# Kernel optimization log

Hardware: AMD Instinct MI355X
Metric: run time of the kernel (lower is better)

Reference implementation:

```python
import jax, jax.numpy as jnp
import numpy as np

# Conv2d_mvm config (matches init_kwargs): the bit-sliced crossbar MVM is a
# fixed-point emulation of an exact stride-1 conv2d with padding=1, no bias.
C_IN, C_OUT, K, H, W, PAD = 16, 16, 3, 1024, 1024, 1


def setup_inputs() -> dict:
    key = jax.random.key(0)
    kx, kw = jax.random.split(key)
    x = jax.random.normal(kx, (1, C_IN, H, W), dtype=jnp.float32)
    # kaiming_uniform-style init for the conv weight
    fan_in = C_IN * K * K
    bound = 1.0 / np.sqrt(fan_in)
    weight = jax.random.uniform(kw, (C_OUT, C_IN, K, K), dtype=jnp.float32,
                                minval=-bound, maxval=bound)
    return {"x": x, "weight": weight}


def reference(x, weight):
    # Ideal math of the bit-sliced crossbar MVM: per output pixel, the
    # flattened (C_in*K*K) receptive field dotted with each flattened filter.
    out = jax.lax.conv_general_dilated(
        x, weight,
        window_strides=(1, 1),
        padding=((PAD, PAD), (PAD, PAD)),
        dimension_numbers=("NCHW", "OIHW", "NCHW"),
    )
    # Original forward returns (C_out, H_out, W_out) with batch=1 assumed.
    return out[0]
```

## Files before the change

kernel.cpp:

```cpp
#include <hip/hip_runtime.h>


#define H 1024
#define W 1024
#define HW (H * W)
#define TW 64
#define TH 8
#define NT 2
#define LROWS 10
#define LPITCH 2112
#define LDS_BYTES (LROWS * LPITCH)

typedef __bf16 bf16x8 __attribute__((ext_vector_type(8)));
typedef float f32x4 __attribute__((ext_vector_type(4)));
typedef unsigned short ushort8 __attribute__((ext_vector_type(8)));
typedef unsigned int uint4v __attribute__((ext_vector_type(4)));

__device__ __host__ inline unsigned short f2bf(float f) {
  unsigned u = __builtin_bit_cast(unsigned, f);
  return (unsigned short)((u + 0x7fffu + ((u >> 16) & 1u)) >> 16);
}

__global__ __launch_bounds__(256) void conv_prep(const float* __restrict__ w,
                                                 unsigned short* __restrict__ wA) {
  int i = blockIdx.x * 256 + threadIdx.x;
  if (i >= 5 * 64 * 8) return;
  int j = i & 7;
  int l = (i >> 3) & 63;
  int p = i >> 9;
  int k = (l >> 4) * 8 + j;
  int t = 2 * p + (k >> 4);
  int ci = k & 15;
  int co = l & 15;
  float v = (t <= 8) ? w[co * 144 + ci * 9 + t] : 0.f;
  wA[i] = f2bf(v);
}

__global__ __launch_bounds__(256, 4) void conv_mfma(
    const float* __restrict__ x, const unsigned short* __restrict__ wA,
    float* __restrict__ out) {
  __shared__ __align__(16) char lds[LDS_BYTES];

  const int tid  = threadIdx.x;
  const int lane = tid & 63;
  const int wave = tid >> 6;
  const int m = lane & 15;
  const int q = lane >> 4;
  const int colbase  = blockIdx.x * TW;
  const int rowbase0 = blockIdx.y * (TH * NT);

  const bool stager = tid < 180;
  int ly = 0;
  const float* xcol = x;
  float cmask[4];
  int lok[4], lb[4];
  if (stager) {
    ly = tid / 18;
    const int qx  = tid - ly * 18;
    const int gx0 = colbase - 4 + 4 * qx;
    const int gx0c = gx0 < 0 ? 0 : (gx0 > W - 4 ? W - 4 : gx0);
    xcol = x + gx0c;
#pragma unroll
    for (int i = 0; i < 4; ++i) {
      const int gx = gx0 + i;
      cmask[i] = ((unsigned)gx < (unsigned)W) ? 1.f : 0.f;
      const int lx = gx - (colbase - 1);
      lok[i] = (unsigned)lx < 66u;
      const int b = ly * LPITCH + lx * 32;
      lb[i] = b ^ (((lx >> 2) & 3) << 4);
    }
  }

  f32x4 L[16];
  float rowm;
  {
    const int gy = rowbase0 - 1 + ly;
    rowm = ((unsigned)gy < (unsigned)H) ? 1.f : 0.f;
    const int gyc = gy < 0 ? 0 : (gy > H - 1 ? H - 1 : gy);
    const float* xb = xcol + gyc * W;
    if (stager) {
#pragma unroll
      for (int c = 0; c < 16; ++c)
        L[c] = *(const f32x4*)(xb + c * HW);
    }
  }

  ushort8 wU[5];
#pragma unroll
  for (int p = 0; p < 5; ++p)
    wU[p] = *(const ushort8*)&wA[(p * 64 + lane) * 8];

  int baseaddr[5];
#pragma unroll
  for (int p = 0; p < 5; ++p) {
    int t = 2 * p + (q >> 1);
    int ky = 0, kx = 0;
    if (t <= 8) { ky = t / 3; kx = t - ky * 3; }
    int col = m + kx;
    int b = ky * LPITCH + col * 32 + (q & 1) * 16;
    b ^= ((col >> 2) & 3) << 4;
    baseaddr[p] = b + wave * 2 * LPITCH;
  }

#pragma unroll
  for (int t = 0; t < NT; ++t) {
    if (stager) {
#pragma unroll
      for (int h = 0; h < 2; ++h) {
#pragma unroll
        for (int i = 0; i < 4; ++i) {
          if (lok[i]) {
            const float fm = rowm * cmask[i];
            uint4v d;
#pragma unroll
            for (int p = 0; p < 4; ++p) {
              const unsigned lo = f2bf(L[h * 8 + 2 * p][i] * fm);
              const unsigned hi = f2bf(L[h * 8 + 2 * p + 1][i] * fm);
              d[p] = lo | (hi << 16);
            }
            *(uint4v*)(lds + (lb[i] ^ (h << 4)));
            *(uint4v*)(lds + (lb[i] ^ (h << 4))) = d;
          }
        }
      }
    }

    if (t + 1 < NT) {
      const int gy = rowbase0 + (t + 1) * TH - 1 + ly;
      const float nrowm = ((unsigned)gy < (unsigned)H) ? 1.f : 0.f;
      const int gyc = gy < 0 ? 0 : (gy > H - 1 ? H - 1 : gy);
      const float* xb = xcol + gyc * W;
      if (stager) {
#pragma unroll
        for (int c = 0; c < 16; ++c)
          L[c] = *(const f32x4*)(xb + c * HW);
      }
      rowm = nrowm;
    }

    __syncthreads();

    const int rowbase = rowbase0 + t * TH;
#pragma unroll
    for (int r = 0; r < 2; ++r) {
#pragma unroll
      for (int g = 0; g < 4; ++g) {
        f32x4 acc = {0.f, 0.f, 0.f, 0.f};
#pragma unroll
        for (int p = 0; p < 5; ++p) {
          ushort8 bU = *(const ushort8*)(lds + (baseaddr[p] + r * LPITCH + g * 512));
          acc = __builtin_amdgcn_mfma_f32_16x16x32_bf16(
              __builtin_bit_cast(bf16x8, bU),
              __builtin_bit_cast(bf16x8, wU[p]),
              acc, 0, 0, 0);
        }
        const int y  = rowbase + wave * 2 + r;
        const int x0 = colbase + g * 16 + q * 4;
        *(f32x4*)(out + m * HW + y * W + x0) = acc;
      }
    }

    if (t + 1 < NT) __syncthreads();
  }
}

extern "C" void kernel_launch(void* const* d_in, const int* in_sizes, int n_in,
                              void* d_out, int out_size, void* d_ws, size_t ws_size,
                              hipStream_t stream) {
  const float* x = (const float*)d_in[0];
  const float* w = (const float*)d_in[1];
  float* out = (float*)d_out;
  unsigned short* wA = (unsigned short*)d_ws;

  conv_prep<<<10, 256, 0, stream>>>(w, wA);

  dim3 grid(W / TW, H / (TH * NT));
  conv_mfma<<<grid, 256, 0, stream>>>(x, wA, out);
}
```

Before: 44.40 us.

## Double-buffer LDS and register prefetch to overlap global loads with MFMA

Each block now processes four row tiles instead of two and keeps two LDS buffers and two register sets for staged input. The load of the next tile is issued before the current tile is converted and written to LDS, and the second barrier per iteration is removed. The plain __syncthreads is swapped for a raw lgkmcnt wait plus s_barrier, so outstanding global loads no longer stall the barrier. The intent is to hide global-load latency and cut synchronisation. The cost is more registers and twice the LDS, which lowers occupancy (launch bounds go from 4 to 2 blocks) and halves the grid size.

Result: slower. 46.39 us (+4.5%).

```diff
diff --git a/kernel.cpp b/kernel.cpp
--- a/kernel.cpp
+++ b/kernel.cpp
@@ -6,10 +6,11 @@
 #define HW (H * W)
 #define TW 64
 #define TH 8
-#define NT 2
+#define NT 4
 #define LROWS 10
 #define LPITCH 2112
-#define LDS_BYTES (LROWS * LPITCH)
+#define LDS_TILE (LROWS * LPITCH)
+#define LDS_BYTES (2 * LDS_TILE)
 
 typedef __bf16 bf16x8 __attribute__((ext_vector_type(8)));
 typedef float f32x4 __attribute__((ext_vector_type(4)));
@@ -36,7 +37,7 @@
   wA[i] = f2bf(v);
 }
 
-__global__ __launch_bounds__(256, 4) void conv_mfma(
+__global__ __launch_bounds__(256, 2) void conv_mfma(
     const float* __restrict__ x, const unsigned short* __restrict__ wA,
     float* __restrict__ out) {
   __shared__ __align__(16) char lds[LDS_BYTES];
@@ -71,17 +72,18 @@
     }
   }
 
-  f32x4 L[16];
-  float rowm;
+  f32x4 L[2][16];
+  float rowm[2];
+
   {
     const int gy = rowbase0 - 1 + ly;
-    rowm = ((unsigned)gy < (unsigned)H) ? 1.f : 0.f;
+    rowm[0] = ((unsigned)gy < (unsigned)H) ? 1.f : 0.f;
     const int gyc = gy < 0 ? 0 : (gy > H - 1 ? H - 1 : gy);
     const float* xb = xcol + gyc * W;
     if (stager) {
 #pragma unroll
       for (int c = 0; c < 16; ++c)
-        L[c] = *(const f32x4*)(xb + c * HW);
+        L[0][c] = *(const f32x4*)(xb + c * HW);
     }
   }
 
@@ -104,43 +106,46 @@
 
 #pragma unroll
   for (int t = 0; t < NT; ++t) {
+    const int cur = t & 1, nxt = cur ^ 1;
+
+    if (t + 1 < NT) {
+      const int gy = rowbase0 + (t + 1) * TH - 1 + ly;
+      rowm[nxt] = ((unsigned)gy < (unsigned)H) ? 1.f : 0.f;
+      const int gyc = gy < 0 ? 0 : (gy > H - 1 ? H - 1 : gy);
+      const float* xb = xcol + gyc * W;
+      if (stager) {
+#pragma unroll
+        for (int c = 0; c < 16; ++c)
+          L[nxt][c] = *(const f32x4*)(xb + c * HW);
+      }
+    }
+
     if (stager) {
+      char* const tb = lds + cur * LDS_TILE;
 #pragma unroll
       for (int h = 0; h < 2; ++h) {
 #pragma unroll
         for (int i = 0; i < 4; ++i) {
           if (lok[i]) {
-            const float fm = rowm * cmask[i];
+            const float fm = rowm[cur] * cmask[i];
             uint4v d;
 #pragma unroll
             for (int p = 0; p < 4; ++p) {
-              const unsigned lo = f2bf(L[h * 8 + 2 * p][i] * fm);
-              const unsigned hi = f2bf(L[h * 8 + 2 * p + 1][i] * fm);
+              const unsigned lo = f2bf(L[cur][h * 8 + 2 * p][i] * fm);
+              const unsigned hi = f2bf(L[cur][h * 8 + 2 * p + 1][i] * fm);
               d[p] = lo | (hi << 16);
             }
-            *(uint4v*)(lds + (lb[i] ^ (h << 4)));
-            *(uint4v*)(lds + (lb[i] ^ (h << 4))) = d;
+            *(uint4v*)(tb + (lb[i] ^ (h << 4))) = d;
           }
         }
       }
     }
 
-    if (t + 1 < NT) {
-      const int gy = rowbase0 + (t + 1) * TH - 1 + ly;
-      const float nrowm = ((unsigned)gy < (unsigned)H) ? 1.f : 0.f;
-      const int gyc = gy < 0 ? 0 : (gy > H - 1 ? H - 1 : gy);
-      const float* xb = xcol + gyc * W;
-      if (stager) {
-#pragma unroll
-        for (int c = 0; c < 16; ++c)
-          L[c] = *(const f32x4*)(xb + c * HW);
-      }
-      rowm = nrowm;
-    }
-
-    __syncthreads();
+    asm volatile("s_waitcnt lgkmcnt(0)" ::: "memory");
+    asm volatile("s_barrier" ::: "memory");
 
     const int rowbase = rowbase0 + t * TH;
+    const char* const bufp = lds + cur * LDS_TILE;
 #pragma unroll
     for (int r = 0; r < 2; ++r) {
 #pragma unroll
@@ -148,7 +153,7 @@
         f32x4 acc = {0.f, 0.f, 0.f, 0.f};
 #pragma unroll
         for (int p = 0; p < 5; ++p) {
-          ushort8 bU = *(const ushort8*)(lds + (baseaddr[p] + r * LPITCH + g * 512));
+          ushort8 bU = *(const ushort8*)(bufp + baseaddr[p] + r * LPITCH + g * 512);
           acc = __builtin_amdgcn_mfma_f32_16x16x32_bf16(
               __builtin_bit_cast(bf16x8, bU),
               __builtin_bit_cast(bf16x8, wU[p]),
@@ -159,8 +164,6 @@
         *(f32x4*)(out + m * HW + y * W + x0) = acc;
       }
     }
-
-    if (t + 1 < NT) __syncthreads();
   }
 }
 
```
